# Optimization experiments

Measured on AMD Instinct MI355X. Metric: run time of the kernel, lower is better.

The kernel has to match this reference:

```python
import jax, jax.numpy as jnp
import numpy as np

Q = 127.0  # 2**(8-1) - 1 signed levels for n_bits=8
EPS = 1e-8


def _ste_fake_quant(x_norm):
    """Clamp to [-1,1], round to Q levels with straight-through estimator."""
    x_c = jnp.clip(x_norm, -1.0, 1.0)
    q = jnp.round(x_c * Q) / Q
    return x_c + jax.lax.stop_gradient(q - x_c)


def setup_inputs() -> dict:
    key = jax.random.key(0)
    ks = jax.random.split(key, 5)
    T, D_in, D_out, R = 16384, 4096, 4096, 32
    x = jax.random.normal(ks[0], (T, D_in), dtype=jnp.float32)
    W = jax.random.normal(ks[1], (D_out, D_in), dtype=jnp.float32) * 0.02
    loraA_w = jax.random.normal(ks[2], (R, D_in), dtype=jnp.float32) * 0.02
    loraB_w = jax.random.normal(ks[3], (D_out, R), dtype=jnp.float32) * 0.02
    bias = jax.random.normal(ks[4], (D_out,), dtype=jnp.float32)
    a_x = jnp.ones((), dtype=jnp.float32)
    return {"x": x, "W": W, "loraA_w": loraA_w, "loraB_w": loraB_w,
            "bias": bias, "a_x": a_x}


def reference(x, W, loraA_w, loraB_w, bias, a_x):
    # 1) LoRA merge: original code runs loraB(loraA(eye(in))).T == B @ A;
    #    we compose the low-rank factors directly (same math, no identity).
    weight_eff = W + loraB_w @ loraA_w                      # [out, in]
    # 2) activation fake-quant with per-step scale a_x (clamped >= eps)
    a_x = jnp.maximum(a_x, EPS)
    x_norm = _ste_fake_quant(x / a_x)                       # [T, in]
    # 3) per-out-channel absmax (detached) + normalized weight fake-quant
    a_w = jax.lax.stop_gradient(
        jnp.max(jnp.abs(weight_eff), axis=1, keepdims=True) + EPS)  # [out,1]
    w_norm = _ste_fake_quant(weight_eff / a_w)              # [out, in]
    # 4) normalized GEMM
    y_norm = x_norm @ w_norm.T                              # [T, out]
    # 5) rescale + 6) FP32 bias add
    out = y_norm * (a_x * a_w).reshape(1, -1) + bias.reshape(1, -1)
    return out
```

## Files before the change

kernel.cpp:

```cpp
#include <hip/hip_runtime.h>
#include <hip/hip_bf16.h>

constexpr int TDIM = 16384;
constexpr int DIN  = 4096;
constexpr int DOUT = 4096;
constexpr int RNK  = 32;
constexpr float EPSF = 1e-8f;

using i32x4 = __attribute__((ext_vector_type(4))) int;

__global__ __launch_bounds__(256)
void wquant_kernel(const float* __restrict__ W,
                   const float* __restrict__ Amat,
                   const float* __restrict__ Bmat,
                   float* __restrict__ a_w,
                   signed char* __restrict__ qw)
{
    const int tid = threadIdx.x;
    const int o0  = blockIdx.x * 4;

    __shared__ float Bsh[4][32];
    __shared__ float red[4][4];
    __shared__ float awsh[4];

    if (tid < 128) {
        int r = tid >> 5, c = tid & 31;
        Bsh[r][c] = Bmat[(size_t)(o0 + r) * RNK + c];
    }
    __syncthreads();

    float4 acc[4][4];
    #pragma unroll
    for (int r = 0; r < 4; ++r)
        #pragma unroll
        for (int c = 0; c < 4; ++c)
            acc[r][c] = *(const float4*)(W + (size_t)(o0 + r) * DIN + c * 1024 + tid * 4);

    #pragma unroll 4
    for (int k = 0; k < RNK; ++k) {
        float4 a[4];
        #pragma unroll
        for (int c = 0; c < 4; ++c)
            a[c] = *(const float4*)(Amat + (size_t)k * DIN + c * 1024 + tid * 4);
        #pragma unroll
        for (int r = 0; r < 4; ++r) {
            const float b = Bsh[r][k];
            #pragma unroll
            for (int c = 0; c < 4; ++c) {
                acc[r][c].x += b * a[c].x; acc[r][c].y += b * a[c].y;
                acc[r][c].z += b * a[c].z; acc[r][c].w += b * a[c].w;
            }
        }
    }

    const int wid = tid >> 6;
    #pragma unroll
    for (int r = 0; r < 4; ++r) {
        float m = 0.f;
        #pragma unroll
        for (int c = 0; c < 4; ++c) {
            float4 v = acc[r][c];
            m = fmaxf(m, fmaxf(fmaxf(fabsf(v.x), fabsf(v.y)),
                               fmaxf(fabsf(v.z), fabsf(v.w))));
        }
        for (int off = 1; off < 64; off <<= 1)
            m = fmaxf(m, __shfl_xor(m, off));
        if ((tid & 63) == 0) red[wid][r] = m;
    }
    __syncthreads();
    if (tid < 4) {
        float m = fmaxf(fmaxf(red[0][tid], red[1][tid]),
                        fmaxf(red[2][tid], red[3][tid]));
        float aw = m + EPSF;
        awsh[tid] = aw;
        a_w[o0 + tid] = aw;
    }
    __syncthreads();

    #pragma unroll
    for (int r = 0; r < 4; ++r) {
        const float aw = awsh[r];
        #pragma unroll
        for (int c = 0; c < 4; ++c) {
            float4 v = acc[r][c];
            int q0 = __float2int_rn((v.x / aw) * 127.0f);
            int q1 = __float2int_rn((v.y / aw) * 127.0f);
            int q2 = __float2int_rn((v.z / aw) * 127.0f);
            int q3 = __float2int_rn((v.w / aw) * 127.0f);
            unsigned int packed = (q0 & 0xff) | ((q1 & 0xff) << 8) |
                                  ((q2 & 0xff) << 16) | ((q3 & 0xff) << 24);
            *(unsigned int*)(qw + (size_t)(o0 + r) * DIN + c * 1024 + tid * 4) = packed;
        }
    }
}

__global__ __launch_bounds__(256)
void xquant_kernel(const float* __restrict__ x,
                   const float* __restrict__ axp,
                   unsigned int* __restrict__ qx)
{
    const float inv = 1.0f / fmaxf(axp[0], EPSF);
    const size_t base = (size_t)blockIdx.x * 1024 + threadIdx.x;
    const float4* xv = (const float4*)x;

    float4 v[4];
    #pragma unroll
    for (int j = 0; j < 4; ++j)
        v[j] = xv[base + j * 256];

    #pragma unroll
    for (int j = 0; j < 4; ++j) {
        int q0 = __float2int_rn(fminf(fmaxf(v[j].x * inv, -1.f), 1.f) * 127.0f);
        int q1 = __float2int_rn(fminf(fmaxf(v[j].y * inv, -1.f), 1.f) * 127.0f);
        int q2 = __float2int_rn(fminf(fmaxf(v[j].z * inv, -1.f), 1.f) * 127.0f);
        int q3 = __float2int_rn(fminf(fmaxf(v[j].w * inv, -1.f), 1.f) * 127.0f);
        qx[base + j * 256] = (q0 & 0xff) | ((q1 & 0xff) << 8) |
                             ((q2 & 0xff) << 16) | ((q3 & 0xff) << 24);
    }
}

__global__ __launch_bounds__(256, 2)
void gemm_i8_kernel(const signed char* __restrict__ qx,
                    const signed char* __restrict__ qw,
                    const float* __restrict__ a_w,
                    const float* __restrict__ bias,
                    const float* __restrict__ axp,
                    float* __restrict__ out)
{
    __shared__ signed char As[128 * 64];
    __shared__ signed char Bs[128 * 64];

    const int tid  = threadIdx.x;
    const int lane = tid & 63;
    const int wid  = tid >> 6;
    const int wm   = wid >> 1;
    const int wn   = wid & 1;

    const int bid = blockIdx.x;
    const int nb  = bid & 31;
    const int mb  = bid >> 5;

    const size_t K = DIN;

    const int srow = tid >> 2;
    const int skb  = tid & 3;
    const int ssw  = (srow ^ (srow >> 2)) & 3;
    const int skb2 = skb ^ ssw;

    const signed char* aSrc = qx + (size_t)(mb * 128) * K;
    const signed char* bSrc = qw + (size_t)(nb * 128) * K;

    const int r15 = lane & 15;
    const int rsw = (r15 ^ (r15 >> 2)) & 3;
    const int rkb = (((lane >> 4) ^ rsw) << 4);
    const int aRdBase = (wm * 64 + r15) * 64 + rkb;
    const int bRdBase = (wn * 64 + r15) * 64 + rkb;

    i32x4 zero = {0, 0, 0, 0};
    i32x4 acc[4][4];
    #pragma unroll
    for (int m = 0; m < 4; ++m)
        #pragma unroll
        for (int n = 0; n < 4; ++n) acc[m][n] = zero;

    for (int kt = 0; kt < (int)(K / 64); ++kt) {
        const size_t kOff = (size_t)kt * 64;
        #pragma unroll
        for (int j = 0; j < 2; ++j) {
            const int row = j * 64 + srow;
            __builtin_amdgcn_global_load_lds(
                (const __attribute__((address_space(1))) unsigned int*)
                    (aSrc + (size_t)row * K + kOff + skb2 * 16),
                (__attribute__((address_space(3))) unsigned int*)
                    (As + j * 4096 + tid * 16),
                16, 0, 0);
        }
        #pragma unroll
        for (int j = 0; j < 2; ++j) {
            const int row = j * 64 + srow;
            __builtin_amdgcn_global_load_lds(
                (const __attribute__((address_space(1))) unsigned int*)
                    (bSrc + (size_t)row * K + kOff + skb2 * 16),
                (__attribute__((address_space(3))) unsigned int*)
                    (Bs + j * 4096 + tid * 16),
                16, 0, 0);
        }
        __syncthreads();

        i32x4 af[4], bf[4];
        #pragma unroll
        for (int m = 0; m < 4; ++m)
            af[m] = *(const i32x4*)(As + aRdBase + m * 1024);
        #pragma unroll
        for (int n = 0; n < 4; ++n)
            bf[n] = *(const i32x4*)(Bs + bRdBase + n * 1024);

        #pragma unroll
        for (int m = 0; m < 4; ++m)
            #pragma unroll
            for (int n = 0; n < 4; ++n)
                acc[m][n] = __builtin_amdgcn_mfma_i32_16x16x64_i8(
                    af[m], bf[n], acc[m][n], 0, 0, 0);

        __syncthreads();
    }

    const float ax = fmaxf(axp[0], EPSF);
    #pragma unroll
    for (int n = 0; n < 4; ++n) {
        const int o = nb * 128 + wn * 64 + n * 16 + r15;
        const float scale = ax * a_w[o] * (1.0f / 16129.0f);
        const float bs = bias[o];
        #pragma unroll
        for (int m = 0; m < 4; ++m) {
            const int t0 = mb * 128 + wm * 64 + m * 16 + ((lane >> 4) << 2);
            float* op = out + (size_t)t0 * DOUT + o;
            #pragma unroll
            for (int r = 0; r < 4; ++r)
                op[(size_t)r * DOUT] = (float)acc[m][n][r] * scale + bs;
        }
    }
}

extern "C" void kernel_launch(void* const* d_in, const int* in_sizes, int n_in,
                              void* d_out, int out_size, void* d_ws, size_t ws_size,
                              hipStream_t stream)
{
    const float* x    = (const float*)d_in[0];
    const float* W    = (const float*)d_in[1];
    const float* lA   = (const float*)d_in[2];
    const float* lB   = (const float*)d_in[3];
    const float* bias = (const float*)d_in[4];
    const float* ax   = (const float*)d_in[5];
    float* out        = (float*)d_out;

    signed char* qx = (signed char*)d_ws;
    signed char* qw = qx + (size_t)TDIM * DIN;
    float* a_w      = (float*)(qw + (size_t)DOUT * DIN);

    wquant_kernel<<<DOUT / 4, 256, 0, stream>>>(W, lA, lB, a_w, qw);

    const int xblocks = (int)(((size_t)TDIM * DIN) / (16 * 256));
    xquant_kernel<<<xblocks, 256, 0, stream>>>(x, ax, (unsigned int*)qx);

    gemm_i8_kernel<<<(TDIM / 128) * (DOUT / 128), 256, 0, stream>>>(
        qx, qw, a_w, bias, ax, out);
}
```

Measured before the change: 457.0 us.

## Enlarge int8 GEMM tile to 256x256 with triple-buffered LDS pipeline

Result: slower. 511.6 us (+11.9%).

```diff
diff --git a/kernel.cpp b/kernel.cpp
--- a/kernel.cpp
+++ b/kernel.cpp
@@ -119,7 +119,7 @@
     }
 }
 
-__global__ __launch_bounds__(256, 2)
+__global__ __launch_bounds__(512, 2)
 void gemm_i8_kernel(const signed char* __restrict__ qx,
                     const signed char* __restrict__ qw,
                     const float* __restrict__ a_w,
@@ -127,93 +127,124 @@
                     const float* __restrict__ axp,
                     float* __restrict__ out)
 {
-    __shared__ signed char As[128 * 64];
-    __shared__ signed char Bs[128 * 64];
+    __shared__ signed char As[3][256 * 64];
+    __shared__ signed char Bs[3][256 * 64];
 
     const int tid  = threadIdx.x;
     const int lane = tid & 63;
     const int wid  = tid >> 6;
-    const int wm   = wid >> 1;
-    const int wn   = wid & 1;
+    const int wm   = wid >> 2;
+    const int wn   = wid & 3;
 
     const int bid = blockIdx.x;
-    const int nb  = bid & 31;
-    const int mb  = bid >> 5;
+    const int nb  = bid & 15;
+    const int mb  = bid >> 4;
 
     const size_t K = DIN;
+    constexpr int NT = DIN / 64;
 
     const int srow = tid >> 2;
-    const int skb  = tid & 3;
-    const int ssw  = (srow ^ (srow >> 2)) & 3;
-    const int skb2 = skb ^ ssw;
-
-    const signed char* aSrc = qx + (size_t)(mb * 128) * K;
-    const signed char* bSrc = qw + (size_t)(nb * 128) * K;
-
-    const int r15 = lane & 15;
-    const int rsw = (r15 ^ (r15 >> 2)) & 3;
-    const int rkb = (((lane >> 4) ^ rsw) << 4);
-    const int aRdBase = (wm * 64 + r15) * 64 + rkb;
-    const int bRdBase = (wn * 64 + r15) * 64 + rkb;
-
-    i32x4 zero = {0, 0, 0, 0};
-    i32x4 acc[4][4];
-    #pragma unroll
-    for (int m = 0; m < 4; ++m)
-        #pragma unroll
-        for (int n = 0; n < 4; ++n) acc[m][n] = zero;
-
-    for (int kt = 0; kt < (int)(K / 64); ++kt) {
-        const size_t kOff = (size_t)kt * 64;
-        #pragma unroll
-        for (int j = 0; j < 2; ++j) {
-            const int row = j * 64 + srow;
-            __builtin_amdgcn_global_load_lds(
-                (const __attribute__((address_space(1))) unsigned int*)
-                    (aSrc + (size_t)row * K + kOff + skb2 * 16),
-                (__attribute__((address_space(3))) unsigned int*)
-                    (As + j * 4096 + tid * 16),
-                16, 0, 0);
-        }
-        #pragma unroll
-        for (int j = 0; j < 2; ++j) {
-            const int row = j * 64 + srow;
-            __builtin_amdgcn_global_load_lds(
-                (const __attribute__((address_space(1))) unsigned int*)
-                    (bSrc + (size_t)row * K + kOff + skb2 * 16),
-                (__attribute__((address_space(3))) unsigned int*)
-                    (Bs + j * 4096 + tid * 16),
-                16, 0, 0);
-        }
-        __syncthreads();
+    const int skb  = ((tid & 3) ^ ((srow >> 1) & 3)) << 4;
+    const signed char* aPanel = qx + (size_t)(mb * 256) * K;
+    const signed char* bPanel = qw + (size_t)(nb * 256) * K;
+
+    const int r15  = lane & 15;
+    const int blk  = lane >> 4;
+    const int rkey = (r15 >> 1) & 3;
+    const int rblk = (blk ^ rkey) << 4;
+    const int aRd  = (wm * 128 + r15) * 64 + rblk;
+    const int bRd  = (wn * 64 + r15) * 64 + rblk;
+
+    i32x4 acc[8][4];
+    #pragma unroll
+    for (int m = 0; m < 8; ++m)
+        #pragma unroll
+        for (int n = 0; n < 4; ++n) acc[m][n] = i32x4{0, 0, 0, 0};
+
+#define STAGE(panel, ldsbuf, tt)                                               \
+    {                                                                          \
+        const int tc = (tt) < NT ? (tt) : (NT - 1);                            \
+        const size_t kOff = (size_t)tc * 64;                                   \
+        _Pragma("unroll")                                                      \
+        for (int j = 0; j < 2; ++j) {                                          \
+            const int row = j * 128 + srow;                                    \
+            __builtin_amdgcn_global_load_lds(                                  \
+                (const __attribute__((address_space(1))) unsigned int*)        \
+                    ((panel) + (size_t)row * K + kOff + skb),                  \
+                (__attribute__((address_space(3))) unsigned int*)              \
+                    ((ldsbuf) + j * 8192 + tid * 16),                          \
+                16, 0, 0);                                                     \
+        }                                                                      \
+    }
+
+    STAGE(aPanel, As[0], 0);
+    STAGE(bPanel, Bs[0], 0);
+    STAGE(aPanel, As[1], 1);
+    STAGE(bPanel, Bs[1], 1);
+    asm volatile("s_waitcnt vmcnt(4)" ::: "memory");
+    __builtin_amdgcn_sched_barrier(0);
+    __builtin_amdgcn_s_barrier();
+
+    for (int t = 0; t < NT; ++t) {
+        const int cur = t % 3;
+        const int nxt = (t + 2) % 3;
+        const signed char* Ab = As[cur];
+        const signed char* Bb = Bs[cur];
 
         i32x4 af[4], bf[4];
         #pragma unroll
         for (int m = 0; m < 4; ++m)
-            af[m] = *(const i32x4*)(As + aRdBase + m * 1024);
+            af[m] = *(const i32x4*)(Ab + aRd + m * 1024);
         #pragma unroll
         for (int n = 0; n < 4; ++n)
-            bf[n] = *(const i32x4*)(Bs + bRdBase + n * 1024);
-
+            bf[n] = *(const i32x4*)(Bb + bRd + n * 1024);
+        STAGE(aPanel, As[nxt], t + 2);
+        __builtin_amdgcn_s_barrier();
+        asm volatile("s_waitcnt lgkmcnt(0)" ::: "memory");
+        __builtin_amdgcn_sched_barrier(0);
+        __builtin_amdgcn_s_setprio(1);
         #pragma unroll
         for (int m = 0; m < 4; ++m)
             #pragma unroll
             for (int n = 0; n < 4; ++n)
                 acc[m][n] = __builtin_amdgcn_mfma_i32_16x16x64_i8(
                     af[m], bf[n], acc[m][n], 0, 0, 0);
-
-        __syncthreads();
-    }
+        __builtin_amdgcn_s_setprio(0);
+        __builtin_amdgcn_sched_barrier(0);
+        __builtin_amdgcn_s_barrier();
+
+        i32x4 ag[4];
+        #pragma unroll
+        for (int m = 0; m < 4; ++m)
+            ag[m] = *(const i32x4*)(Ab + aRd + (m + 4) * 1024);
+        STAGE(bPanel, Bs[nxt], t + 2);
+        __builtin_amdgcn_s_barrier();
+        asm volatile("s_waitcnt lgkmcnt(0)" ::: "memory");
+        __builtin_amdgcn_sched_barrier(0);
+        __builtin_amdgcn_s_setprio(1);
+        #pragma unroll
+        for (int m = 0; m < 4; ++m)
+            #pragma unroll
+            for (int n = 0; n < 4; ++n)
+                acc[m + 4][n] = __builtin_amdgcn_mfma_i32_16x16x64_i8(
+                    ag[m], bf[n], acc[m + 4][n], 0, 0, 0);
+        __builtin_amdgcn_s_setprio(0);
+        __builtin_amdgcn_sched_barrier(0);
+        asm volatile("s_waitcnt vmcnt(4)" ::: "memory");
+        __builtin_amdgcn_sched_barrier(0);
+        __builtin_amdgcn_s_barrier();
+    }
+#undef STAGE
 
     const float ax = fmaxf(axp[0], EPSF);
     #pragma unroll
     for (int n = 0; n < 4; ++n) {
-        const int o = nb * 128 + wn * 64 + n * 16 + r15;
+        const int o = nb * 256 + wn * 64 + n * 16 + r15;
         const float scale = ax * a_w[o] * (1.0f / 16129.0f);
         const float bs = bias[o];
         #pragma unroll
-        for (int m = 0; m < 4; ++m) {
-            const int t0 = mb * 128 + wm * 64 + m * 16 + ((lane >> 4) << 2);
+        for (int m = 0; m < 8; ++m) {
+            const int t0 = mb * 256 + wm * 128 + m * 16 + (blk << 2);
             float* op = out + (size_t)t0 * DOUT + o;
             #pragma unroll
             for (int r = 0; r < 4; ++r)
@@ -243,6 +274,6 @@
     const int xblocks = (int)(((size_t)TDIM * DIN) / (16 * 256));
     xquant_kernel<<<xblocks, 256, 0, stream>>>(x, ax, (unsigned int*)qx);
 
-    gemm_i8_kernel<<<(TDIM / 128) * (DOUT / 128), 256, 0, stream>>>(
+    gemm_i8_kernel<<<(TDIM / 256) * (DOUT / 256), 512, 0, stream>>>(
         qx, qw, a_w, bias, ax, out);
 }
```

## Add 256x256 double-buffered int8 GEMM kernel for half of the token rows

Applied to the files above, without the earlier changes.

Measured after the change: 462.5 us. About the same (+1.2%).

```diff
diff --git a/kernel.cpp b/kernel.cpp
--- a/kernel.cpp
+++ b/kernel.cpp
@@ -119,13 +119,178 @@
     }
 }
 
+__global__ __launch_bounds__(512, 2)
+void gemm8_kernel(const signed char* __restrict__ qx,
+                  const signed char* __restrict__ qw,
+                  const float* __restrict__ a_w,
+                  const float* __restrict__ bias,
+                  const float* __restrict__ axp,
+                  float* __restrict__ out)
+{
+    __shared__ signed char As[2 * 256 * 128];
+    __shared__ signed char Bs[2 * 256 * 128];
+
+    const int tid  = threadIdx.x;
+    const int lane = tid & 63;
+    const int wid  = tid >> 6;
+    const int wm   = wid >> 2;
+    const int wn   = wid & 3;
+
+    const int bid = blockIdx.x;
+    const int nb  = bid & 15;
+    const int mb  = bid >> 4;
+
+    const size_t K = DIN;
+    constexpr int NT = DIN / 128;
+
+    const int srow8 = tid >> 3;
+    const int sblk  = ((tid & 7) ^ ((tid >> 4) & 7)) << 4;
+    const signed char* aPanel = qx + (size_t)(mb * 256) * K;
+    const signed char* bPanel = qw + (size_t)(nb * 256) * K;
+
+    const int r15  = lane & 15;
+    const int blk  = lane >> 4;
+    const int key  = (r15 >> 1) & 7;
+    const int sw0  = (blk ^ key) << 4;
+    const int sw1  = ((blk ^ key) ^ 4) << 4;
+    const int aRd0 = (wm * 128 + r15) * 128 + sw0;
+    const int aRd1 = (wm * 128 + r15) * 128 + sw1;
+    const int bRd0 = (wn * 64 + r15) * 128 + sw0;
+    const int bRd1 = (wn * 64 + r15) * 128 + sw1;
+
+    i32x4 acc[8][4];
+    #pragma unroll
+    for (int m = 0; m < 8; ++m)
+        #pragma unroll
+        for (int n = 0; n < 4; ++n) acc[m][n] = i32x4{0, 0, 0, 0};
+
+#define STAGE_U(panel, ldsArr, T, h, pb)                                       \
+    {                                                                          \
+        const int tc = (T) < NT ? (T) : (NT - 1);                              \
+        const size_t kOff = (size_t)tc * 128;                                  \
+        _Pragma("unroll")                                                      \
+        for (int j = 0; j < 2; ++j) {                                          \
+            __builtin_amdgcn_global_load_lds(                                  \
+                (const __attribute__((address_space(1))) unsigned int*)        \
+                    ((panel) + (size_t)((h) * 128 + j * 64 + srow8) * K + kOff + sblk), \
+                (__attribute__((address_space(3))) unsigned int*)              \
+                    ((ldsArr) + (pb) * 32768 + (h) * 16384 + j * 8192 + tid * 16), \
+                16, 0, 0);                                                     \
+        }                                                                      \
+    }
+
+    STAGE_U(bPanel, Bs, 0, 0, 0); STAGE_U(bPanel, Bs, 0, 1, 0);
+    STAGE_U(aPanel, As, 0, 0, 0); STAGE_U(aPanel, As, 0, 1, 0);
+    STAGE_U(bPanel, Bs, 1, 0, 1); STAGE_U(bPanel, Bs, 1, 1, 1);
+    asm volatile("s_waitcnt vmcnt(4)" ::: "memory");
+    __builtin_amdgcn_sched_barrier(0);
+    __builtin_amdgcn_s_barrier();
+
+    for (int t = 0; t < NT; ++t) {
+        const int p = t & 1;
+        const signed char* Ab = As + p * 32768;
+        const signed char* Bb = Bs + p * 32768;
+        i32x4 bf0[4], bf1[4], af[4];
+
+        #pragma unroll
+        for (int n = 0; n < 4; ++n) bf0[n] = *(const i32x4*)(Bb + bRd0 + n * 2048);
+        #pragma unroll
+        for (int m = 0; m < 4; ++m) af[m] = *(const i32x4*)(Ab + aRd0 + m * 2048);
+        STAGE_U(aPanel, As, t + 1, 0, p ^ 1);
+        __builtin_amdgcn_s_barrier();
+        asm volatile("s_waitcnt lgkmcnt(0)" ::: "memory");
+        __builtin_amdgcn_sched_barrier(0);
+        __builtin_amdgcn_s_setprio(1);
+        #pragma unroll
+        for (int m = 0; m < 4; ++m)
+            #pragma unroll
+            for (int n = 0; n < 4; ++n)
+                acc[m][n] = __builtin_amdgcn_mfma_i32_16x16x64_i8(af[m], bf0[n], acc[m][n], 0, 0, 0);
+        __builtin_amdgcn_s_setprio(0);
+        __builtin_amdgcn_sched_barrier(0);
+        __builtin_amdgcn_s_barrier();
+
+        #pragma unroll
+        for (int n = 0; n < 4; ++n) bf1[n] = *(const i32x4*)(Bb + bRd1 + n * 2048);
+        #pragma unroll
+        for (int m = 0; m < 4; ++m) af[m] = *(const i32x4*)(Ab + aRd1 + m * 2048);
+        STAGE_U(aPanel, As, t + 1, 1, p ^ 1);
+        __builtin_amdgcn_s_barrier();
+        asm volatile("s_waitcnt lgkmcnt(0)" ::: "memory");
+        __builtin_amdgcn_sched_barrier(0);
+        __builtin_amdgcn_s_setprio(1);
+        #pragma unroll
+        for (int m = 0; m < 4; ++m)
+            #pragma unroll
+            for (int n = 0; n < 4; ++n)
+                acc[m][n] = __builtin_amdgcn_mfma_i32_16x16x64_i8(af[m], bf1[n], acc[m][n], 0, 0, 0);
+        __builtin_amdgcn_s_setprio(0);
+        __builtin_amdgcn_sched_barrier(0);
+        __builtin_amdgcn_s_barrier();
+
+        #pragma unroll
+        for (int m = 0; m < 4; ++m) af[m] = *(const i32x4*)(Ab + aRd0 + 8192 + m * 2048);
+        STAGE_U(bPanel, Bs, t + 2, 0, p);
+        __builtin_amdgcn_s_barrier();
+        asm volatile("s_waitcnt lgkmcnt(0)" ::: "memory");
+        __builtin_amdgcn_sched_barrier(0);
+        __builtin_amdgcn_s_setprio(1);
+        #pragma unroll
+        for (int m = 0; m < 4; ++m)
+            #pragma unroll
+            for (int n = 0; n < 4; ++n)
+                acc[m + 4][n] = __builtin_amdgcn_mfma_i32_16x16x64_i8(af[m], bf0[n], acc[m + 4][n], 0, 0, 0);
+        __builtin_amdgcn_s_setprio(0);
+        __builtin_amdgcn_sched_barrier(0);
+        __builtin_amdgcn_s_barrier();
+
+        #pragma unroll
+        for (int m = 0; m < 4; ++m) af[m] = *(const i32x4*)(Ab + aRd1 + 8192 + m * 2048);
+        STAGE_U(bPanel, Bs, t + 2, 1, p);
+        __builtin_amdgcn_s_barrier();
+        asm volatile("s_waitcnt lgkmcnt(0)" ::: "memory");
+        __builtin_amdgcn_sched_barrier(0);
+        __builtin_amdgcn_s_setprio(1);
+        #pragma unroll
+        for (int m = 0; m < 4; ++m)
+            #pragma unroll
+            for (int n = 0; n < 4; ++n)
+                acc[m + 4][n] = __builtin_amdgcn_mfma_i32_16x16x64_i8(af[m], bf1[n], acc[m + 4][n], 0, 0, 0);
+        __builtin_amdgcn_s_setprio(0);
+        __builtin_amdgcn_sched_barrier(0);
+        asm volatile("s_waitcnt vmcnt(4)" ::: "memory");
+        __builtin_amdgcn_sched_barrier(0);
+        __builtin_amdgcn_s_barrier();
+    }
+#undef STAGE_U
+
+    asm volatile("s_waitcnt vmcnt(0)" ::: "memory");
+
+    const float ax = fmaxf(axp[0], EPSF);
+    #pragma unroll
+    for (int n = 0; n < 4; ++n) {
+        const int o = nb * 256 + wn * 64 + n * 16 + r15;
+        const float scale = ax * a_w[o] * (1.0f / 16129.0f);
+        const float bs = bias[o];
+        #pragma unroll
+        for (int m = 0; m < 8; ++m) {
+            const int t0 = mb * 256 + wm * 128 + m * 16 + (blk << 2);
+            float* op = out + (size_t)t0 * DOUT + o;
+            #pragma unroll
+            for (int r = 0; r < 4; ++r)
+                op[(size_t)r * DOUT] = (float)acc[m][n][r] * scale + bs;
+        }
+    }
+}
+
 __global__ __launch_bounds__(256, 2)
-void gemm_i8_kernel(const signed char* __restrict__ qx,
-                    const signed char* __restrict__ qw,
-                    const float* __restrict__ a_w,
-                    const float* __restrict__ bias,
-                    const float* __restrict__ axp,
-                    float* __restrict__ out)
+void gemm97_kernel(const signed char* __restrict__ qx,
+                   const signed char* __restrict__ qw,
+                   const float* __restrict__ a_w,
+                   const float* __restrict__ bias,
+                   const float* __restrict__ axp,
+                   float* __restrict__ out,
+                   int mBase)
 {
     __shared__ signed char As[128 * 64];
     __shared__ signed char Bs[128 * 64];
@@ -147,7 +312,7 @@
     const int ssw  = (srow ^ (srow >> 2)) & 3;
     const int skb2 = skb ^ ssw;
 
-    const signed char* aSrc = qx + (size_t)(mb * 128) * K;
+    const signed char* aSrc = qx + (size_t)(mBase + mb * 128) * K;
     const signed char* bSrc = qw + (size_t)(nb * 128) * K;
 
     const int r15 = lane & 15;
@@ -156,12 +321,11 @@
     const int aRdBase = (wm * 64 + r15) * 64 + rkb;
     const int bRdBase = (wn * 64 + r15) * 64 + rkb;
 
-    i32x4 zero = {0, 0, 0, 0};
     i32x4 acc[4][4];
     #pragma unroll
     for (int m = 0; m < 4; ++m)
         #pragma unroll
-        for (int n = 0; n < 4; ++n) acc[m][n] = zero;
+        for (int n = 0; n < 4; ++n) acc[m][n] = i32x4{0, 0, 0, 0};
 
     for (int kt = 0; kt < (int)(K / 64); ++kt) {
         const size_t kOff = (size_t)kt * 64;
@@ -213,7 +377,7 @@
         const float bs = bias[o];
         #pragma unroll
         for (int m = 0; m < 4; ++m) {
-            const int t0 = mb * 128 + wm * 64 + m * 16 + ((lane >> 4) << 2);
+            const int t0 = mBase + mb * 128 + wm * 64 + m * 16 + ((lane >> 4) << 2);
             float* op = out + (size_t)t0 * DOUT + o;
             #pragma unroll
             for (int r = 0; r < 4; ++r)
@@ -243,6 +407,8 @@
     const int xblocks = (int)(((size_t)TDIM * DIN) / (16 * 256));
     xquant_kernel<<<xblocks, 256, 0, stream>>>(x, ax, (unsigned int*)qx);
 
-    gemm_i8_kernel<<<(TDIM / 128) * (DOUT / 128), 256, 0, stream>>>(
+    gemm8_kernel<<<(8192 / 256) * (DOUT / 256), 512, 0, stream>>>(
         qx, qw, a_w, bias, ax, out);
+    gemm97_kernel<<<(8192 / 128) * (DOUT / 128), 256, 0, stream>>>(
+        qx, qw, a_w, bias, ax, out, 8192);
 }
```
